# Kernel optimization log

Hardware: AMD Instinct MI355X
Metric: run time of the kernel (lower is better)

Reference implementation:

```python
import jax, jax.numpy as jnp
import numpy as np

D_MODEL = 1024
N_HEADS = 16
D_K = D_MODEL // N_HEADS


def setup_inputs() -> dict:
    key = jax.random.key(0)
    ks = jax.random.split(key, 5)
    scale = 1.0 / np.sqrt(D_MODEL)
    x = jax.random.normal(ks[0], (4, 2048, D_MODEL), dtype=jnp.float32)
    W_Q = jax.random.uniform(ks[1], (D_MODEL, D_MODEL), jnp.float32, -scale, scale)
    W_K = jax.random.uniform(ks[2], (D_MODEL, D_MODEL), jnp.float32, -scale, scale)
    W_V = jax.random.uniform(ks[3], (D_MODEL, D_MODEL), jnp.float32, -scale, scale)
    W_O = jax.random.uniform(ks[4], (D_MODEL, D_MODEL), jnp.float32, -scale, scale)
    return {"x": x, "W_Q": W_Q, "W_K": W_K, "W_V": W_V, "W_O": W_O}


def reference(x, W_Q, W_K, W_V, W_O):
    B, S, _ = x.shape
    # nn.Linear(y) = y @ W.T ; weights stored (out, in)
    def heads(W):
        return jnp.einsum('bsd,ed->bse', x, W).reshape(B, S, N_HEADS, D_K).transpose(0, 2, 1, 3)
    Q, K, V = heads(W_Q), heads(W_K), heads(W_V)  # [B,H,S,Dk]
    scores = jnp.einsum('bhqd,bhkd->bhqk', Q, K) / np.sqrt(D_K)
    causal = jnp.tril(jnp.ones((S, S), dtype=bool))
    scores = jnp.where(causal[None, None], scores, -jnp.inf)
    attn = jax.nn.softmax(scores, axis=-1)  # [B,H,S,S]
    out = jnp.einsum('bhqk,bhkd->bhqd', attn, V)
    out = out.transpose(0, 2, 1, 3).reshape(B, S, D_MODEL)
    return jnp.einsum('bsd,ed->bse', out, W_O)
```

## Files before the change

kernel.cpp:

```cpp
#include <hip/hip_runtime.h>
#include <hip/hip_bf16.h>
#include <stdint.h>

#define D_MODEL 1024
#define NHEADS  16
#define DKH     64
#define BATCH   4
#define SEQ     2048
#define NTOK    (BATCH * SEQ)

typedef unsigned short u16;
using bf16x8 = __attribute__((ext_vector_type(8))) short;
using f32x4  = __attribute__((ext_vector_type(4))) float;
using f32x16 = __attribute__((ext_vector_type(16))) float;
using u32x2  = __attribute__((ext_vector_type(2))) unsigned int;

#define GLD16(g, l)                                                            \
  __builtin_amdgcn_global_load_lds(                                            \
      (const __attribute__((address_space(1))) void*)(g),                      \
      (__attribute__((address_space(3))) void*)(l), 16, 0, 0)

__device__ inline u16 f2bf(float f) {
  __hip_bfloat16 h = __float2bfloat16(f);
  return __builtin_bit_cast(u16, h);
}

__device__ inline float fexp2(float x) { return __builtin_amdgcn_exp2f(x); }

__device__ inline unsigned cvtpk(float lo, float hi) {
  unsigned r;
  asm("v_cvt_pk_bf16_f32 %0, %1, %2" : "=v"(r) : "v"(lo), "v"(hi));
  return r;
}

template <int B>
__device__ inline bf16x8 make_pfrag(const f32x16& sv) {
  unsigned x1 = cvtpk(sv[B + 0], sv[B + 1]);
  unsigned y1 = cvtpk(sv[B + 4], sv[B + 5]);
  unsigned x2 = cvtpk(sv[B + 2], sv[B + 3]);
  unsigned y2 = cvtpk(sv[B + 6], sv[B + 7]);
  u32x2 s1 = __builtin_amdgcn_permlane32_swap(x1, y1, false, false);
  u32x2 s2 = __builtin_amdgcn_permlane32_swap(x2, y2, false, false);
  union { unsigned u[4]; bf16x8 v; } r;
  r.u[0] = s1[0]; r.u[1] = s2[0]; r.u[2] = s1[1]; r.u[3] = s2[1];
  return r.v;
}

__global__ __launch_bounds__(256) void cvt_all(const float* __restrict__ x,
                                               const float* __restrict__ wq,
                                               const float* __restrict__ wk,
                                               const float* __restrict__ wv,
                                               const float* __restrict__ wo,
                                               u16* xb, u16* wqb, u16* wkb, u16* wvb, u16* wob) {
  const int XC = NTOK * D_MODEL / 4;
  const int WC = D_MODEL * D_MODEL / 4;
  const int total = XC + 4 * WC;
  for (int i = blockIdx.x * 256 + threadIdx.x; i < total; i += gridDim.x * 256) {
    const float4* s; ushort4* d; int j;
    if (i < XC)              { s = (const float4*)x;  d = (ushort4*)xb;  j = i; }
    else if (i < XC + WC)    { s = (const float4*)wq; d = (ushort4*)wqb; j = i - XC; }
    else if (i < XC + 2*WC)  { s = (const float4*)wk; d = (ushort4*)wkb; j = i - XC - WC; }
    else if (i < XC + 3*WC)  { s = (const float4*)wv; d = (ushort4*)wvb; j = i - XC - 2*WC; }
    else                     { s = (const float4*)wo; d = (ushort4*)wob; j = i - XC - 3*WC; }
    float4 v = s[j];
    d[j] = make_ushort4(f2bf(v.x), f2bf(v.y), f2bf(v.z), f2bf(v.w));
  }
}

__global__ __launch_bounds__(256) void gemm_qkv(const u16* __restrict__ A,
                                                const u16* __restrict__ Bq,
                                                const u16* __restrict__ Bk,
                                                const u16* __restrict__ Bv,
                                                u16* __restrict__ Qo,
                                                u16* __restrict__ Ko,
                                                u16* __restrict__ Vo) {
  __shared__ u16 As[2][128 * 64];
  __shared__ u16 Bs[2][128 * 64];
  const int h = blockIdx.x;
  const int L = (h & 7) * 192 + (h >> 3);
  const int z = L / 512;
  const int rr = L % 512;
  const int bM = (rr >> 3) * 128;
  const int bN = (rr & 7) * 128;
  const u16* __restrict__ Bp = z == 0 ? Bq : (z == 1 ? Bk : Bv);
  const int t = threadIdx.x, lane = t & 63, wave = t >> 6;
  const int wr = wave >> 1, wc = wave & 1;
  const int frow = lane & 15, g = lane >> 4;

  auto stage = [&](int buf, int k0) {
#pragma unroll
    for (int p = 0; p < 4; ++p) {
      int chunk = p * 256 + t;
      int r = chunk >> 3, cc = chunk & 7;
      int cs = cc ^ (r & 7);
      GLD16(A + (size_t)(bM + r) * D_MODEL + k0 + cs * 8, &As[buf][(size_t)(p * 256 + (t & ~63)) * 8]);
      GLD16(Bp + (size_t)(bN + r) * D_MODEL + k0 + cs * 8, &Bs[buf][(size_t)(p * 256 + (t & ~63)) * 8]);
    }
  };

  f32x4 acc[4][4] = {};
  stage(0, 0);
  __syncthreads();

  int cur = 0;
  for (int k0 = 0; k0 < D_MODEL; k0 += 64) {
    if (k0 + 64 < D_MODEL) stage(cur ^ 1, k0 + 64);

    bf16x8 a[2][4], b[2][4];
#pragma unroll
    for (int kk = 0; kk < 2; ++kk) {
#pragma unroll
      for (int m = 0; m < 4; ++m)
        a[kk][m] = *(const bf16x8*)&As[cur][(wr * 64 + m * 16 + frow) * 64 +
                                           (((kk * 4 + g) ^ (frow & 7)) * 8)];
#pragma unroll
      for (int n = 0; n < 4; ++n)
        b[kk][n] = *(const bf16x8*)&Bs[cur][(wc * 64 + n * 16 + frow) * 64 +
                                           (((kk * 4 + g) ^ (frow & 7)) * 8)];
    }
#pragma unroll
    for (int kk = 0; kk < 2; ++kk)
#pragma unroll
      for (int m = 0; m < 4; ++m)
#pragma unroll
        for (int n = 0; n < 4; ++n)
          acc[m][n] = __builtin_amdgcn_mfma_f32_16x16x32_bf16(a[kk][m], b[kk][n], acc[m][n], 0, 0, 0);

    __syncthreads();
    cur ^= 1;
  }

  const int r0 = bM + wr * 64 + (lane >> 4) * 4;
  const int c0 = bN + wc * 64 + (lane & 15);
  if (z == 2) {
#pragma unroll
    for (int m = 0; m < 4; ++m)
#pragma unroll
      for (int n = 0; n < 4; ++n) {
        int r = r0 + m * 16;
        int cc = c0 + n * 16;
        size_t off = ((size_t)(r >> 11) * D_MODEL + cc) * SEQ + (r & (SEQ - 1));
        *(ushort4*)(Vo + off) = make_ushort4(f2bf(acc[m][n][0]), f2bf(acc[m][n][1]),
                                             f2bf(acc[m][n][2]), f2bf(acc[m][n][3]));
      }
  } else {
    u16* C = z ? Ko : Qo;
    const float sc = z ? 1.0f : 0.18033688f;
#pragma unroll
    for (int m = 0; m < 4; ++m)
#pragma unroll
      for (int n = 0; n < 4; ++n)
#pragma unroll
        for (int j = 0; j < 4; ++j)
          C[(size_t)(r0 + m * 16 + j) * D_MODEL + (c0 + n * 16)] = f2bf(acc[m][n][j] * sc);
  }
}

__global__ __launch_bounds__(256) void gemm_out(const u16* __restrict__ A,
                                                const u16* __restrict__ B,
                                                float* __restrict__ C) {
  __shared__ u16 As[2][128 * 64];
  __shared__ u16 Bs[2][128 * 64];
  const int h = blockIdx.x;
  const int L = (h & 7) * 64 + (h >> 3);
  const int bM = (L >> 3) * 128;
  const int bN = (L & 7) * 128;
  const int t = threadIdx.x, lane = t & 63, wave = t >> 6;
  const int wr = wave >> 1, wc = wave & 1;
  const int frow = lane & 15, g = lane >> 4;

  auto stage = [&](int buf, int k0) {
#pragma unroll
    for (int p = 0; p < 4; ++p) {
      int chunk = p * 256 + t;
      int r = chunk >> 3, cc = chunk & 7;
      int cs = cc ^ (r & 7);
      GLD16(A + (size_t)(bM + r) * D_MODEL + k0 + cs * 8, &As[buf][(size_t)(p * 256 + (t & ~63)) * 8]);
      GLD16(B + (size_t)(bN + r) * D_MODEL + k0 + cs * 8, &Bs[buf][(size_t)(p * 256 + (t & ~63)) * 8]);
    }
  };

  f32x4 acc[4][4] = {};
  stage(0, 0);
  __syncthreads();

  int cur = 0;
  for (int k0 = 0; k0 < D_MODEL; k0 += 64) {
    if (k0 + 64 < D_MODEL) stage(cur ^ 1, k0 + 64);

    bf16x8 a[2][4], b[2][4];
#pragma unroll
    for (int kk = 0; kk < 2; ++kk) {
#pragma unroll
      for (int m = 0; m < 4; ++m)
        a[kk][m] = *(const bf16x8*)&As[cur][(wr * 64 + m * 16 + frow) * 64 +
                                           (((kk * 4 + g) ^ (frow & 7)) * 8)];
#pragma unroll
      for (int n = 0; n < 4; ++n)
        b[kk][n] = *(const bf16x8*)&Bs[cur][(wc * 64 + n * 16 + frow) * 64 +
                                           (((kk * 4 + g) ^ (frow & 7)) * 8)];
    }
#pragma unroll
    for (int kk = 0; kk < 2; ++kk)
#pragma unroll
      for (int m = 0; m < 4; ++m)
#pragma unroll
        for (int n = 0; n < 4; ++n)
          acc[m][n] = __builtin_amdgcn_mfma_f32_16x16x32_bf16(a[kk][m], b[kk][n], acc[m][n], 0, 0, 0);

    __syncthreads();
    cur ^= 1;
  }

  const int r0 = bM + wr * 64 + (lane >> 4) * 4;
  const int c0 = bN + wc * 64 + (lane & 15);
#pragma unroll
  for (int m = 0; m < 4; ++m)
#pragma unroll
    for (int n = 0; n < 4; ++n)
#pragma unroll
      for (int j = 0; j < 4; ++j)
        C[(size_t)(r0 + m * 16 + j) * D_MODEL + (c0 + n * 16)] = acc[m][n][j];
}

__global__ __launch_bounds__(256) void attn_fwd(const u16* __restrict__ Q,
                                                const u16* __restrict__ K,
                                                const u16* __restrict__ Vt,
                                                u16* __restrict__ O) {
  __shared__ u16 Kl[2][64 * 64];
  __shared__ u16 Vl[2][64 * 64];
  const int t = threadIdx.x, lane = t & 63, wave = t >> 6;
  const int q = lane & 31, hi = lane >> 5;
  const int bh = blockIdx.x & 63;
  const int p = blockIdx.x >> 6;
  const size_t rowbase = (size_t)(bh >> 4) * SEQ;
  const int hcol = (bh & 15) * DKH;
  const size_t vbase = (size_t)bh * DKH;

  auto stage = [&](int buf, int kv0) {
#pragma unroll
    for (int pp = 0; pp < 2; ++pp) {
      int chunk = pp * 256 + t;
      int r = chunk >> 3, cc = chunk & 7;
      int cs = cc ^ (r & 7);
      GLD16(K + (rowbase + kv0 + r) * D_MODEL + hcol + cs * 8,
            &Kl[buf][(size_t)(pp * 256 + (t & ~63)) * 8]);
      GLD16(Vt + (vbase + r) * SEQ + kv0 + cs * 8,
            &Vl[buf][(size_t)(pp * 256 + (t & ~63)) * 8]);
    }
  };

#pragma unroll 1
  for (int item = 0; item < 2; ++item) {
    const int qtile = item ? p : 15 - p;
    const int q0 = qtile * 128;
    const int qw = q0 + wave * 32;
    const int nit = qtile * 2 + 2;

    stage(0, 0);

    bf16x8 qf[4];
#pragma unroll
    for (int w = 0; w < 4; ++w)
      qf[w] = *(const bf16x8*)&Q[(rowbase + qw + q) * D_MODEL + hcol + w * 16 + hi * 8];

    f32x16 ot0 = {}, ot1 = {};
    float mstate = -__builtin_inff();
    float lstate = 0.f;

    __syncthreads();
    int cur = 0;
    for (int it = 0; it < nit; ++it) {
      const int kv0 = it * 64;
      if (it + 1 < nit) stage(cur ^ 1, kv0 + 64);

      if (kv0 <= qw + 31) {
        f32x16 s0 = {}, s1 = {};
        __builtin_amdgcn_s_setprio(1);
#pragma unroll
        for (int w = 0; w < 4; ++w) {
          const int rk0 = q, rk1 = 32 + q;
          bf16x8 k0 = *(const bf16x8*)&Kl[cur][rk0 * 64 + (((2 * w + hi) ^ (rk0 & 7)) * 8)];
          bf16x8 k1 = *(const bf16x8*)&Kl[cur][rk1 * 64 + (((2 * w + hi) ^ (rk0 & 7)) * 8)];
          s0 = __builtin_amdgcn_mfma_f32_32x32x16_bf16(k0, qf[w], s0, 0, 0, 0);
          s1 = __builtin_amdgcn_mfma_f32_32x32x16_bf16(k1, qf[w], s1, 0, 0, 0);
        }
        __builtin_amdgcn_s_setprio(0);

        const int qg = qw + q;
        if (kv0 + 63 > qw) {
#pragma unroll
          for (int r = 0; r < 16; ++r) {
            const int crow = (r & 3) + 8 * (r >> 2) + 4 * hi;
            if (kv0 + crow > qg) s0[r] = -__builtin_inff();
            if (kv0 + 32 + crow > qg) s1[r] = -__builtin_inff();
          }
        }

        float pmax = fmaxf(s0[0], s0[1]);
#pragma unroll
        for (int r = 2; r < 16; ++r) pmax = fmaxf(pmax, s0[r]);
#pragma unroll
        for (int r = 0; r < 16; ++r) pmax = fmaxf(pmax, s1[r]);
        pmax = fmaxf(pmax, __shfl_xor(pmax, 32));

        if (__any(pmax > mstate + 11.5416f)) {
          float mnew = fmaxf(mstate, pmax);
          float al = fexp2(mstate - mnew);
          mstate = mnew;
          lstate *= al;
#pragma unroll
          for (int r = 0; r < 16; ++r) { ot0[r] *= al; ot1[r] *= al; }
        }
        const float mm = mstate;

        float lsum = 0.f;
#pragma unroll
        for (int r = 0; r < 16; ++r) { s0[r] = fexp2(s0[r] - mm); lsum += s0[r]; }
#pragma unroll
        for (int r = 0; r < 16; ++r) { s1[r] = fexp2(s1[r] - mm); lsum += s1[r]; }
        lsum += __shfl_xor(lsum, 32);
        lstate += lsum;

        bf16x8 pb0 = make_pfrag<0>(s0);
        bf16x8 pb1 = make_pfrag<8>(s0);
        bf16x8 pb2 = make_pfrag<0>(s1);
        bf16x8 pb3 = make_pfrag<8>(s1);

        __builtin_amdgcn_s_setprio(1);
#define PV_STEP(KB, PB)                                                                   \
        {                                                                                 \
          bf16x8 v0 = *(const bf16x8*)&Vl[cur][q * 64 + (((2 * (KB) + hi) ^ (q & 7)) * 8)]; \
          bf16x8 v1 = *(const bf16x8*)&Vl[cur][(32 + q) * 64 + (((2 * (KB) + hi) ^ (q & 7)) * 8)]; \
          ot0 = __builtin_amdgcn_mfma_f32_32x32x16_bf16(v0, PB, ot0, 0, 0, 0);            \
          ot1 = __builtin_amdgcn_mfma_f32_32x32x16_bf16(v1, PB, ot1, 0, 0, 0);            \
        }
        PV_STEP(0, pb0)
        PV_STEP(1, pb1)
        PV_STEP(2, pb2)
        PV_STEP(3, pb3)
#undef PV_STEP
        __builtin_amdgcn_s_setprio(0);
      }
      __syncthreads();
      cur ^= 1;
    }

    const float inv = 1.0f / lstate;
    u16* orow = &O[(rowbase + qw + q) * D_MODEL + hcol];
#pragma unroll
    for (int g2 = 0; g2 < 4; ++g2) {
      ushort4 a4 = make_ushort4(f2bf(ot0[4 * g2 + 0] * inv), f2bf(ot0[4 * g2 + 1] * inv),
                                f2bf(ot0[4 * g2 + 2] * inv), f2bf(ot0[4 * g2 + 3] * inv));
      *(ushort4*)&orow[8 * g2 + 4 * hi] = a4;
      ushort4 b4 = make_ushort4(f2bf(ot1[4 * g2 + 0] * inv), f2bf(ot1[4 * g2 + 1] * inv),
                                f2bf(ot1[4 * g2 + 2] * inv), f2bf(ot1[4 * g2 + 3] * inv));
      *(ushort4*)&orow[32 + 8 * g2 + 4 * hi] = b4;
    }
  }
}

extern "C" void kernel_launch(void* const* d_in, const int* in_sizes, int n_in,
                              void* d_out, int out_size, void* d_ws, size_t ws_size,
                              hipStream_t stream) {
  const float* x  = (const float*)d_in[0];
  const float* Wq = (const float*)d_in[1];
  const float* Wk = (const float*)d_in[2];
  const float* Wv = (const float*)d_in[3];
  const float* Wo = (const float*)d_in[4];
  float* out = (float*)d_out;

  u16* ws  = (u16*)d_ws;
  u16* xb  = ws;
  u16* wqb = xb + (size_t)NTOK * D_MODEL;
  u16* wkb = wqb + (size_t)D_MODEL * D_MODEL;
  u16* wvb = wkb + (size_t)D_MODEL * D_MODEL;
  u16* wob = wvb + (size_t)D_MODEL * D_MODEL;
  u16* Qb  = wob + (size_t)D_MODEL * D_MODEL;
  u16* Kb  = Qb + (size_t)NTOK * D_MODEL;
  u16* Vb  = Kb + (size_t)NTOK * D_MODEL;
  u16* Ob  = xb;

  cvt_all<<<2048, 256, 0, stream>>>(x, Wq, Wk, Wv, Wo, xb, wqb, wkb, wvb, wob);

  gemm_qkv<<<1536, 256, 0, stream>>>(xb, wqb, wkb, wvb, Qb, Kb, Vb);

  attn_fwd<<<512, 256, 0, stream>>>(Qb, Kb, Vb, Ob);

  gemm_out<<<512, 256, 0, stream>>>(Ob, wob, out);
}
```

Baseline: 166.7 us.

## Process two interleaved 32-row query chains per wave sharing K/V fragments

```diff
diff --git a/kernel.cpp b/kernel.cpp
--- a/kernel.cpp
+++ b/kernel.cpp
@@ -232,10 +232,15 @@
   const int t = threadIdx.x, lane = t & 63, wave = t >> 6;
   const int q = lane & 31, hi = lane >> 5;
   const int bh = blockIdx.x & 63;
-  const int p = blockIdx.x >> 6;
+  const int jj = blockIdx.x >> 6;
+  const int T = jj < 4 ? 7 - jj : jj - 4;
+  const int q0 = T * 256;
   const size_t rowbase = (size_t)(bh >> 4) * SEQ;
   const int hcol = (bh & 15) * DKH;
   const size_t vbase = (size_t)bh * DKH;
+  const int qA = q0 + wave * 32;
+  const int qB = qA + 128;
+  const int nit = 4 * T + 4;
 
   auto stage = [&](int buf, int kv0) {
 #pragma unroll
@@ -250,111 +255,137 @@
     }
   };
 
-#pragma unroll 1
-  for (int item = 0; item < 2; ++item) {
-    const int qtile = item ? p : 15 - p;
-    const int q0 = qtile * 128;
-    const int qw = q0 + wave * 32;
-    const int nit = qtile * 2 + 2;
-
-    stage(0, 0);
-
-    bf16x8 qf[4];
-#pragma unroll
-    for (int w = 0; w < 4; ++w)
-      qf[w] = *(const bf16x8*)&Q[(rowbase + qw + q) * D_MODEL + hcol + w * 16 + hi * 8];
-
-    f32x16 ot0 = {}, ot1 = {};
-    float mstate = -__builtin_inff();
-    float lstate = 0.f;
+  stage(0, 0);
+
+  bf16x8 qa[4], qb[4];
+#pragma unroll
+  for (int w = 0; w < 4; ++w) {
+    qa[w] = *(const bf16x8*)&Q[(rowbase + qA + q) * D_MODEL + hcol + w * 16 + hi * 8];
+    qb[w] = *(const bf16x8*)&Q[(rowbase + qB + q) * D_MODEL + hcol + w * 16 + hi * 8];
+  }
+
+  f32x16 oA0 = {}, oA1 = {}, oB0 = {}, oB1 = {};
+  float mA = -__builtin_inff(), lA = 0.f;
+  float mB = -__builtin_inff(), lB = 0.f;
+
+  __syncthreads();
+  int cur = 0;
+  for (int it = 0; it < nit; ++it) {
+    const int kv0 = it * 64;
+    if (it + 1 < nit) stage(cur ^ 1, kv0 + 64);
+
+    const bool actA = kv0 <= qA + 31;
+    const bool actB = kv0 <= qB + 31;
+
+    bf16x8 k0f[4], k1f[4];
+#pragma unroll
+    for (int w = 0; w < 4; ++w) {
+      k0f[w] = *(const bf16x8*)&Kl[cur][q * 64 + (((2 * w + hi) ^ (q & 7)) * 8)];
+      k1f[w] = *(const bf16x8*)&Kl[cur][(32 + q) * 64 + (((2 * w + hi) ^ (q & 7)) * 8)];
+    }
+
+    f32x16 sA0 = {}, sA1 = {}, sB0 = {}, sB1 = {};
+    __builtin_amdgcn_s_setprio(1);
+#pragma unroll
+    for (int w = 0; w < 4; ++w) {
+      if (actA) {
+        sA0 = __builtin_amdgcn_mfma_f32_32x32x16_bf16(k0f[w], qa[w], sA0, 0, 0, 0);
+        sA1 = __builtin_amdgcn_mfma_f32_32x32x16_bf16(k1f[w], qa[w], sA1, 0, 0, 0);
+      }
+      if (actB) {
+        sB0 = __builtin_amdgcn_mfma_f32_32x32x16_bf16(k0f[w], qb[w], sB0, 0, 0, 0);
+        sB1 = __builtin_amdgcn_mfma_f32_32x32x16_bf16(k1f[w], qb[w], sB1, 0, 0, 0);
+      }
+    }
+    __builtin_amdgcn_s_setprio(0);
+
+    bf16x8 v0f[4], v1f[4];
+#pragma unroll
+    for (int kb = 0; kb < 4; ++kb) {
+      v0f[kb] = *(const bf16x8*)&Vl[cur][q * 64 + (((2 * kb + hi) ^ (q & 7)) * 8)];
+      v1f[kb] = *(const bf16x8*)&Vl[cur][(32 + q) * 64 + (((2 * kb + hi) ^ (q & 7)) * 8)];
+    }
+
+#define CHAIN_STEP(S0, S1, MST, LST, OT0, OT1, QW)                                   \
+    {                                                                                \
+      const int qg = (QW) + q;                                                       \
+      if (kv0 + 63 > (QW)) {                                                         \
+        _Pragma("unroll")                                                            \
+        for (int r = 0; r < 16; ++r) {                                               \
+          const int crow = (r & 3) + 8 * (r >> 2) + 4 * hi;                          \
+          if (kv0 + crow > qg) S0[r] = -__builtin_inff();                            \
+          if (kv0 + 32 + crow > qg) S1[r] = -__builtin_inff();                       \
+        }                                                                            \
+      }                                                                              \
+      float pmax = fmaxf(S0[0], S0[1]);                                              \
+      _Pragma("unroll")                                                              \
+      for (int r = 2; r < 16; ++r) pmax = fmaxf(pmax, S0[r]);                        \
+      _Pragma("unroll")                                                              \
+      for (int r = 0; r < 16; ++r) pmax = fmaxf(pmax, S1[r]);                        \
+      pmax = fmaxf(pmax, __shfl_xor(pmax, 32));                                      \
+      if (__any(pmax > MST + 11.5416f)) {                                            \
+        float mnew = fmaxf(MST, pmax);                                               \
+        float al = fexp2(MST - mnew);                                                \
+        MST = mnew;                                                                  \
+        LST *= al;                                                                   \
+        _Pragma("unroll")                                                            \
+        for (int r = 0; r < 16; ++r) { OT0[r] *= al; OT1[r] *= al; }                 \
+      }                                                                              \
+      const float mm = MST;                                                          \
+      float lsum = 0.f;                                                              \
+      _Pragma("unroll")                                                              \
+      for (int r = 0; r < 16; ++r) { S0[r] = fexp2(S0[r] - mm); lsum += S0[r]; }     \
+      _Pragma("unroll")                                                              \
+      for (int r = 0; r < 16; ++r) { S1[r] = fexp2(S1[r] - mm); lsum += S1[r]; }     \
+      lsum += __shfl_xor(lsum, 32);                                                  \
+      LST += lsum;                                                                   \
+      bf16x8 pb0 = make_pfrag<0>(S0);                                                \
+      bf16x8 pb1 = make_pfrag<8>(S0);                                                \
+      bf16x8 pb2 = make_pfrag<0>(S1);                                                \
+      bf16x8 pb3 = make_pfrag<8>(S1);                                                \
+      __builtin_amdgcn_s_setprio(1);                                                 \
+      OT0 = __builtin_amdgcn_mfma_f32_32x32x16_bf16(v0f[0], pb0, OT0, 0, 0, 0);      \
+      OT1 = __builtin_amdgcn_mfma_f32_32x32x16_bf16(v1f[0], pb0, OT1, 0, 0, 0);      \
+      OT0 = __builtin_amdgcn_mfma_f32_32x32x16_bf16(v0f[1], pb1, OT0, 0, 0, 0);      \
+      OT1 = __builtin_amdgcn_mfma_f32_32x32x16_bf16(v1f[1], pb1, OT1, 0, 0, 0);      \
+      OT0 = __builtin_amdgcn_mfma_f32_32x32x16_bf16(v0f[2], pb2, OT0, 0, 0, 0);      \
+      OT1 = __builtin_amdgcn_mfma_f32_32x32x16_bf16(v1f[2], pb2, OT1, 0, 0, 0);      \
+      OT0 = __builtin_amdgcn_mfma_f32_32x32x16_bf16(v0f[3], pb3, OT0, 0, 0, 0);      \
+      OT1 = __builtin_amdgcn_mfma_f32_32x32x16_bf16(v1f[3], pb3, OT1, 0, 0, 0);      \
+      __builtin_amdgcn_s_setprio(0);                                                 \
+    }
+
+    if (actA) CHAIN_STEP(sA0, sA1, mA, lA, oA0, oA1, qA)
+    if (actB) CHAIN_STEP(sB0, sB1, mB, lB, oB0, oB1, qB)
+#undef CHAIN_STEP
 
     __syncthreads();
-    int cur = 0;
-    for (int it = 0; it < nit; ++it) {
-      const int kv0 = it * 64;
-      if (it + 1 < nit) stage(cur ^ 1, kv0 + 64);
-
-      if (kv0 <= qw + 31) {
-        f32x16 s0 = {}, s1 = {};
-        __builtin_amdgcn_s_setprio(1);
-#pragma unroll
-        for (int w = 0; w < 4; ++w) {
-          const int rk0 = q, rk1 = 32 + q;
-          bf16x8 k0 = *(const bf16x8*)&Kl[cur][rk0 * 64 + (((2 * w + hi) ^ (rk0 & 7)) * 8)];
-          bf16x8 k1 = *(const bf16x8*)&Kl[cur][rk1 * 64 + (((2 * w + hi) ^ (rk0 & 7)) * 8)];
-          s0 = __builtin_amdgcn_mfma_f32_32x32x16_bf16(k0, qf[w], s0, 0, 0, 0);
-          s1 = __builtin_amdgcn_mfma_f32_32x32x16_bf16(k1, qf[w], s1, 0, 0, 0);
-        }
-        __builtin_amdgcn_s_setprio(0);
-
-        const int qg = qw + q;
-        if (kv0 + 63 > qw) {
-#pragma unroll
-          for (int r = 0; r < 16; ++r) {
-            const int crow = (r & 3) + 8 * (r >> 2) + 4 * hi;
-            if (kv0 + crow > qg) s0[r] = -__builtin_inff();
-            if (kv0 + 32 + crow > qg) s1[r] = -__builtin_inff();
-          }
-        }
-
-        float pmax = fmaxf(s0[0], s0[1]);
-#pragma unroll
-        for (int r = 2; r < 16; ++r) pmax = fmaxf(pmax, s0[r]);
-#pragma unroll
-        for (int r = 0; r < 16; ++r) pmax = fmaxf(pmax, s1[r]);
-        pmax = fmaxf(pmax, __shfl_xor(pmax, 32));
-
-        if (__any(pmax > mstate + 11.5416f)) {
-          float mnew = fmaxf(mstate, pmax);
-          float al = fexp2(mstate - mnew);
-          mstate = mnew;
-          lstate *= al;
-#pragma unroll
-          for (int r = 0; r < 16; ++r) { ot0[r] *= al; ot1[r] *= al; }
-        }
-        const float mm = mstate;
-
-        float lsum = 0.f;
-#pragma unroll
-        for (int r = 0; r < 16; ++r) { s0[r] = fexp2(s0[r] - mm); lsum += s0[r]; }
-#pragma unroll
-        for (int r = 0; r < 16; ++r) { s1[r] = fexp2(s1[r] - mm); lsum += s1[r]; }
-        lsum += __shfl_xor(lsum, 32);
-        lstate += lsum;
-
-        bf16x8 pb0 = make_pfrag<0>(s0);
-        bf16x8 pb1 = make_pfrag<8>(s0);
-        bf16x8 pb2 = make_pfrag<0>(s1);
-        bf16x8 pb3 = make_pfrag<8>(s1);
-
-        __builtin_amdgcn_s_setprio(1);
-#define PV_STEP(KB, PB)                                                                   \
-        {                                                                                 \
-          bf16x8 v0 = *(const bf16x8*)&Vl[cur][q * 64 + (((2 * (KB) + hi) ^ (q & 7)) * 8)]; \
-          bf16x8 v1 = *(const bf16x8*)&Vl[cur][(32 + q) * 64 + (((2 * (KB) + hi) ^ (q & 7)) * 8)]; \
-          ot0 = __builtin_amdgcn_mfma_f32_32x32x16_bf16(v0, PB, ot0, 0, 0, 0);            \
-          ot1 = __builtin_amdgcn_mfma_f32_32x32x16_bf16(v1, PB, ot1, 0, 0, 0);            \
-        }
-        PV_STEP(0, pb0)
-        PV_STEP(1, pb1)
-        PV_STEP(2, pb2)
-        PV_STEP(3, pb3)
-#undef PV_STEP
-        __builtin_amdgcn_s_setprio(0);
-      }
-      __syncthreads();
-      cur ^= 1;
-    }
-
-    const float inv = 1.0f / lstate;
-    u16* orow = &O[(rowbase + qw + q) * D_MODEL + hcol];
+    cur ^= 1;
+  }
+
+  {
+    const float invA = 1.0f / lA;
+    u16* orow = &O[(rowbase + qA + q) * D_MODEL + hcol];
 #pragma unroll
     for (int g2 = 0; g2 < 4; ++g2) {
-      ushort4 a4 = make_ushort4(f2bf(ot0[4 * g2 + 0] * inv), f2bf(ot0[4 * g2 + 1] * inv),
-                                f2bf(ot0[4 * g2 + 2] * inv), f2bf(ot0[4 * g2 + 3] * inv));
+      ushort4 a4 = make_ushort4(f2bf(oA0[4 * g2 + 0] * invA), f2bf(oA0[4 * g2 + 1] * invA),
+                                f2bf(oA0[4 * g2 + 2] * invA), f2bf(oA0[4 * g2 + 3] * invA));
       *(ushort4*)&orow[8 * g2 + 4 * hi] = a4;
-      ushort4 b4 = make_ushort4(f2bf(ot1[4 * g2 + 0] * inv), f2bf(ot1[4 * g2 + 1] * inv),
-                                f2bf(ot1[4 * g2 + 2] * inv), f2bf(ot1[4 * g2 + 3] * inv));
+      ushort4 b4 = make_ushort4(f2bf(oA1[4 * g2 + 0] * invA), f2bf(oA1[4 * g2 + 1] * invA),
+                                f2bf(oA1[4 * g2 + 2] * invA), f2bf(oA1[4 * g2 + 3] * invA));
+      *(ushort4*)&orow[32 + 8 * g2 + 4 * hi] = b4;
+    }
+  }
+  {
+    const float invB = 1.0f / lB;
+    u16* orow = &O[(rowbase + qB + q) * D_MODEL + hcol];
+#pragma unroll
+    for (int g2 = 0; g2 < 4; ++g2) {
+      ushort4 a4 = make_ushort4(f2bf(oB0[4 * g2 + 0] * invB), f2bf(oB0[4 * g2 + 1] * invB),
+                                f2bf(oB0[4 * g2 + 2] * invB), f2bf(oB0[4 * g2 + 3] * invB));
+      *(ushort4*)&orow[8 * g2 + 4 * hi] = a4;
+      ushort4 b4 = make_ushort4(f2bf(oB1[4 * g2 + 0] * invB), f2bf(oB1[4 * g2 + 1] * invB),
+                                f2bf(oB1[4 * g2 + 2] * invB), f2bf(oB1[4 * g2 + 3] * invB));
       *(ushort4*)&orow[32 + 8 * g2 + 4 * hi] = b4;
     }
   }
```

Measured after the change: 215.2 us. 1.29x slower.
